# Kernel optimization log

Measured on AMD Instinct MI355X. Metric: run time of the kernel, lower is better.

Reference implementation:

```python
import jax, jax.numpy as jnp
import numpy as np
import math

NUM_SYN = 1000
NUM_MEM = 100
TAU_MIN, TAU_MAX = 10.0, 1000.0
TAU_S = 5.0
DELTA_T = 1.0
LAMBDA = 3.0

def _kappas():
    kappa_s = np.float32(np.exp(-DELTA_T / TAU_S))  # scalar (tau_s uniform)
    tau_m = np.logspace(math.log10(TAU_MIN + 1e-06), math.log10(TAU_MAX - 1e-06), NUM_MEM)
    kappa_m = np.exp(-DELTA_T / np.clip(tau_m, 1e-06, None)).astype(np.float32)
    return kappa_s, jnp.asarray(kappa_m)

def custom_tanh(x):
    return jnp.tanh(x * (2.0 / 3.0)) * 1.7159

def setup_inputs() -> dict:
    key = jax.random.key(0)
    ks = jax.random.split(key, 5)
    B, T = 128, 1024
    H = 2 * NUM_MEM  # 200
    X = jax.random.normal(ks[0], (B, T, NUM_SYN), dtype=jnp.float32)
    w_s = jnp.full((NUM_SYN,), 0.5, dtype=jnp.float32)
    W1 = jax.random.normal(ks[1], (NUM_SYN + NUM_MEM, H), dtype=jnp.float32) * 0.03
    b1 = jnp.zeros((H,), dtype=jnp.float32)
    W2 = jax.random.normal(ks[2], (H, NUM_MEM), dtype=jnp.float32) * 0.07
    b2 = jnp.zeros((NUM_MEM,), dtype=jnp.float32)
    Wy = jax.random.normal(ks[3], (NUM_MEM, 10), dtype=jnp.float32) * 0.1
    by = jnp.zeros((10,), dtype=jnp.float32)
    return {"X": X, "w_s": w_s, "W1": W1, "b1": b1, "W2": W2, "b2": b2, "Wy": Wy, "by": by}

def reference(X, w_s, W1, b1, W2, b2, Wy, by):
    kappa_s, kappa_m = _kappas()
    B = X.shape[0]
    w_s_pos = jax.nn.relu(w_s)

    def step(carry, x_t):
        s, m = carry  # s: [B, S], m: [B, M]
        s = kappa_s * s + w_s_pos * x_t
        km = kappa_m * m
        inp = jnp.concatenate([s, km], axis=-1)  # [B, S+M]
        h = jax.nn.relu(inp @ W1 + b1)
        dm = custom_tanh(h @ W2 + b2)
        m = km + LAMBDA * (1.0 - kappa_m) * dm
        y = m @ Wy + by
        return (s, m), y

    s0 = jnp.zeros((B, NUM_SYN), dtype=X.dtype)
    m0 = jnp.zeros((B, NUM_MEM), dtype=X.dtype)
    Xt = jnp.swapaxes(X, 0, 1)  # [T, B, S]
    _, ys = jax.lax.scan(step, (s0, m0), Xt)
    return jnp.swapaxes(ys, 0, 1)  # [B, T, num_output]
```

## Files before the change

### kernel.cpp

```cpp
#include <hip/hip_runtime.h>
#include <math.h>

#define SDIM 1000
#define KPAD 1024
#define HDIM 200
#define MDIM 100
#define NPAD 208
#define TSTEPS 1024
#define BATCH 128
#define MT (BATCH*TSTEPS)
#define TOTX ((size_t)MT*(size_t)SDIM)

#define Z_OFF 458752

typedef _Float16 half2_t __attribute__((ext_vector_type(2)));
typedef __attribute__((ext_vector_type(8))) short short8;
typedef __attribute__((ext_vector_type(4))) float f32x4;

static __device__ __forceinline__ unsigned short f2bf(float f) {
    unsigned u = __float_as_uint(f);
    unsigned r = 0x7fffu + ((u >> 16) & 1u);
    return (unsigned short)((u + r) >> 16);
}
static __device__ __forceinline__ float bf2f(unsigned short h) {
    return __uint_as_float((unsigned)h << 16);
}
static __device__ __forceinline__ half2_t as_h2(unsigned v) {
    union { unsigned u; half2_t h; } c; c.u = v; return c.h;
}
static __device__ __forceinline__ unsigned as_u32(half2_t h) {
    union { half2_t h; unsigned u; } c; c.h = h; return c.u;
}
static __device__ __forceinline__ half2_t pk2(float a, float b) {
    half2_t r; r[0] = (_Float16)a; r[1] = (_Float16)b; return r;
}

static __device__ __forceinline__ void wg_barrier() {
    asm volatile("s_waitcnt lgkmcnt(0)" ::: "memory");
    __builtin_amdgcn_s_barrier();
    asm volatile("" ::: "memory");
}

__global__ __launch_bounds__(256) void prep_wpt(const float* __restrict__ w_s,
                                                const float* __restrict__ W1,
                                                unsigned short* __restrict__ wpt) {
    int idx = blockIdx.x * 256 + threadIdx.x;
    int n = idx >> 10, k = idx & (KPAD - 1);
    float v = 0.f;
    if (n < HDIM && k < SDIM) {
        float ws = fmaxf(w_s[k], 0.f);
        v = ws * W1[k * HDIM + n];
    }
    wpt[idx] = f2bf(v);
}

__global__ __launch_bounds__(256) void gemm_z(const float* __restrict__ X,
                                              const unsigned short* __restrict__ wpt,
                                              unsigned short* __restrict__ Z) {
    __shared__ __align__(16) unsigned short Abuf[2][128][40];
    __shared__ __align__(16) unsigned short Bbuf[2][13][16][40];
    const int t = threadIdx.x;
    const int m0 = blockIdx.x * 128;
    const int lane = t & 63, w = t >> 6;

    f32x4 acc[2][13];
#pragma unroll
    for (int mt = 0; mt < 2; ++mt)
#pragma unroll
        for (int i = 0; i < 13; ++i) acc[mt][i] = (f32x4){0.f, 0.f, 0.f, 0.f};

    auto stageA = [&](int bsel, int k0) {
        const int row = t >> 1, half = t & 1;
        size_t g = (size_t)(m0 + row) * SDIM + (size_t)(k0 + half * 16);
        float4 f0{}, f1{}, f2{}, f3{};
        if (g + 15 < TOTX) {
            f0 = *(const float4*)(X + g);      f1 = *(const float4*)(X + g + 4);
            f2 = *(const float4*)(X + g + 8);  f3 = *(const float4*)(X + g + 12);
        }
        short8 p0, p1;
        p0[0]=(short)f2bf(f0.x); p0[1]=(short)f2bf(f0.y); p0[2]=(short)f2bf(f0.z); p0[3]=(short)f2bf(f0.w);
        p0[4]=(short)f2bf(f1.x); p0[5]=(short)f2bf(f1.y); p0[6]=(short)f2bf(f1.z); p0[7]=(short)f2bf(f1.w);
        p1[0]=(short)f2bf(f2.x); p1[1]=(short)f2bf(f2.y); p1[2]=(short)f2bf(f2.z); p1[3]=(short)f2bf(f2.w);
        p1[4]=(short)f2bf(f3.x); p1[5]=(short)f2bf(f3.y); p1[6]=(short)f2bf(f3.z); p1[7]=(short)f2bf(f3.w);
        *(short8*)&Abuf[bsel][row][half * 16]     = p0;
        *(short8*)&Abuf[bsel][row][half * 16 + 8] = p1;
    };
    auto stageB = [&](int bsel, int k0) {
#pragma unroll
        for (int j = 0; j < 4; ++j) {
            int e = t + 256 * j;
            if (e < 832) {
                int n = e >> 2, q = e & 3;
                short8 v = *(const short8*)(wpt + (size_t)n * KPAD + k0 + q * 8);
                *(short8*)&Bbuf[bsel][n >> 4][n & 15][q * 8] = v;
            }
        }
    };

    stageA(0, 0);
    stageB(0, 0);
#pragma unroll 1
    for (int it = 0; it < 32; ++it) {
        __syncthreads();
        if (it + 1 < 32) { stageA((it + 1) & 1, (it + 1) * 32); stageB((it + 1) & 1, (it + 1) * 32); }
        const int bsel = it & 1;
        const short8 av0 = *(const short8*)&Abuf[bsel][w * 32 + (lane & 15)][(lane >> 4) * 8];
        const short8 av1 = *(const short8*)&Abuf[bsel][w * 32 + 16 + (lane & 15)][(lane >> 4) * 8];
#pragma unroll
        for (int nt = 0; nt < 13; ++nt) {
            const short8 bv = *(const short8*)&Bbuf[bsel][nt][lane & 15][(lane >> 4) * 8];
            acc[0][nt] = __builtin_amdgcn_mfma_f32_16x16x32_bf16(av0, bv, acc[0][nt], 0, 0, 0);
            acc[1][nt] = __builtin_amdgcn_mfma_f32_16x16x32_bf16(av1, bv, acc[1][nt], 0, 0, 0);
        }
    }

    const int colb = lane & 15;
#pragma unroll
    for (int mt = 0; mt < 2; ++mt) {
        const int rowb = m0 + w * 32 + mt * 16 + (lane >> 4) * 4;
#pragma unroll
        for (int nt = 0; nt < 13; ++nt) {
            int col = nt * 16 + colb;
            if (col < HDIM) {
#pragma unroll
                for (int r = 0; r < 4; ++r)
                    Z[(size_t)(rowb + r) * HDIM + col] = f2bf(acc[mt][nt][r]);
            }
        }
    }
}

#define KEXP 1.9235933878519513f

__global__ __launch_bounds__(256, 1) void scan_seq(const unsigned short* __restrict__ Z,
        const float* __restrict__ W1, const float* __restrict__ b1,
        const float* __restrict__ W2, const float* __restrict__ b2,
        const float* __restrict__ Wy, const float* __restrict__ by,
        float* __restrict__ out) {
    __shared__ __align__(16) float part[2][4][104];
    __shared__ float kap_s[104], cm_s[104];

    const int t = threadIdx.x;
    const int b = blockIdx.x;
    const int w = t >> 6, lane = t & 63;
    const int n = 50 * w + lane;
    const bool hAct = lane < 50;
    const bool yAct = (w == 0) && (lane >= 50 && lane < 60);
    const int o = lane - 50;

    if (t < 104) {
        float kv = 0.f, cv = 0.f;
        if (t < MDIM) {
            double lg = 1.0000000434294482
                      + (double)t * ((2.9999999995657055 - 1.0000000434294482) / 99.0);
            double tau = exp(lg * 2.302585092994046);
            kv = (float)exp(-1.0 / tau);
            cv = 3.0f * (1.0f - kv);
        }
        kap_s[t] = kv; cm_s[t] = cv;
    }
    __syncthreads();

    half2_t w1r[50];
#pragma unroll
    for (int c = 0; c < 50; ++c) {
        float a0 = 0.f, a1 = 0.f;
        if (hAct) {
            a0 = kap_s[2 * c]     * W1[(SDIM + 2 * c)     * HDIM + n];
            a1 = kap_s[2 * c + 1] * W1[(SDIM + 2 * c + 1) * HDIM + n];
        } else if (yAct) {
            a0 = Wy[(2 * c) * 10 + o];
            a1 = Wy[(2 * c + 1) * 10 + o];
        }
        w1r[c] = pk2(a0, a1);
    }
    float base_b = hAct ? b1[n] : (yAct ? by[o] : 0.f);

    const int j0 = 2 * lane, j1 = 2 * lane + 1;
    half2_t w2r[50];
#pragma unroll
    for (int c = 0; c < 25; ++c) {
        float a00 = 0.f, a10 = 0.f, a01 = 0.f, a11 = 0.f;
        if (hAct) {
            int k0 = 50 * w + 2 * c, k1 = k0 + 1;
            a00 = W2[k0 * MDIM + j0]; a10 = W2[k1 * MDIM + j0];
            a01 = W2[k0 * MDIM + j1]; a11 = W2[k1 * MDIM + j1];
        }
        w2r[2 * c]     = pk2(a00, a10);
        w2r[2 * c + 1] = pk2(a01, a11);
    }

    float kap0 = 0.f, kap1 = 0.f, cm0 = 0.f, cm1 = 0.f, b2k0 = 0.f, b2k1 = 0.f;
    if (hAct) {
        kap0 = kap_s[j0]; kap1 = kap_s[j1];
        cm0 = cm_s[j0];   cm1 = cm_s[j1];
        b2k0 = b2[j0] * KEXP;  b2k1 = b2[j1] * KEXP;
    }

    const unsigned short* Zb = Z + (size_t)b * TSTEPS * HDIM;
    float* outb = out + (size_t)b * TSTEPS * 10;

    float u = 0.f, m0 = 0.f, m1 = 0.f;
    unsigned short zA = 0, zB = 0;
    if (hAct) { zA = Zb[n]; zB = Zb[HDIM + n]; }

    int sm[50];
#pragma unroll
    for (int c = 0; c < 50; ++c) sm[c] = 0;

    __syncthreads();

    auto stepf = [&](const int P, unsigned short& zreg, const int st) {
        u = 0.81873075307798182f * u + bf2f(zreg);
        if (hAct) {
            int stn = st + 2; stn = (stn < TSTEPS) ? stn : TSTEPS - 1;
            zreg = Zb[(size_t)stn * HDIM + n];
        }
        float d0 = base_b + u, d1 = 0.f, d2 = 0.f, d3 = 0.f;
#pragma unroll
        for (int c = 0; c < 48; c += 4) {
            d0 = __builtin_amdgcn_fdot2(w1r[c+0], as_h2((unsigned)sm[c+0]), d0, false);
            d1 = __builtin_amdgcn_fdot2(w1r[c+1], as_h2((unsigned)sm[c+1]), d1, false);
            d2 = __builtin_amdgcn_fdot2(w1r[c+2], as_h2((unsigned)sm[c+2]), d2, false);
            d3 = __builtin_amdgcn_fdot2(w1r[c+3], as_h2((unsigned)sm[c+3]), d3, false);
        }
        d0 = __builtin_amdgcn_fdot2(w1r[48], as_h2((unsigned)sm[48]), d0, false);
        d1 = __builtin_amdgcn_fdot2(w1r[49], as_h2((unsigned)sm[49]), d1, false);
        float r = (d0 + d1) + (d2 + d3);
        if (yAct && st > 0) outb[(size_t)(st - 1) * 10 + o] = r;
        float h = fmaxf(r, 0.f);

        float ho = __shfl_xor(h, 1);
        unsigned hpk = as_u32(pk2(h, ho));
        int sh[25];
#pragma unroll
        for (int c = 0; c < 25; ++c) sh[c] = __builtin_amdgcn_readlane((int)hpk, 2 * c);

        if (hAct) {
            float a00 = 0.f, a01 = 0.f, a10 = 0.f, a11 = 0.f;
#pragma unroll
            for (int c = 0; c < 24; c += 2) {
                a00 = __builtin_amdgcn_fdot2(w2r[2*c],   as_h2((unsigned)sh[c]),   a00, false);
                a10 = __builtin_amdgcn_fdot2(w2r[2*c+1], as_h2((unsigned)sh[c]),   a10, false);
                a01 = __builtin_amdgcn_fdot2(w2r[2*c+2], as_h2((unsigned)sh[c+1]), a01, false);
                a11 = __builtin_amdgcn_fdot2(w2r[2*c+3], as_h2((unsigned)sh[c+1]), a11, false);
            }
            a00 = __builtin_amdgcn_fdot2(w2r[48], as_h2((unsigned)sh[24]), a00, false);
            a10 = __builtin_amdgcn_fdot2(w2r[49], as_h2((unsigned)sh[24]), a10, false);
            *(float2*)&part[P][w][j0] = make_float2(a00 + a01, a10 + a11);
        }
        wg_barrier();

        if (hAct) {
            float2 q0 = *(const float2*)&part[P][0][j0];
            float2 q1 = *(const float2*)&part[P][1][j0];
            float2 q2 = *(const float2*)&part[P][2][j0];
            float2 q3 = *(const float2*)&part[P][3][j0];
            float s0 = (q0.x + q1.x) + (q2.x + q3.x);
            float s1 = (q0.y + q1.y) + (q2.y + q3.y);
            float e0 = __builtin_amdgcn_exp2f(fmaf(s0, KEXP, b2k0));
            float e1 = __builtin_amdgcn_exp2f(fmaf(s1, KEXP, b2k1));
            float dm0 = 1.7159f * (1.f - 2.f * __builtin_amdgcn_rcpf(e0 + 1.f));
            float dm1 = 1.7159f * (1.f - 2.f * __builtin_amdgcn_rcpf(e1 + 1.f));
            m0 = fmaf(kap0, m0, cm0 * dm0);
            m1 = fmaf(kap1, m1, cm1 * dm1);
        }
        unsigned mpk = as_u32(pk2(m0, m1));
#pragma unroll
        for (int c = 0; c < 50; ++c) sm[c] = __builtin_amdgcn_readlane((int)mpk, c);
    };

#pragma unroll 1
    for (int st = 0; st < TSTEPS; st += 2) {
        stepf(0, zA, st);
        stepf(1, zB, st + 1);
    }

    if (yAct) {
        float d0 = base_b, d1 = 0.f, d2 = 0.f, d3 = 0.f;
#pragma unroll
        for (int c = 0; c < 48; c += 4) {
            d0 = __builtin_amdgcn_fdot2(w1r[c+0], as_h2((unsigned)sm[c+0]), d0, false);
            d1 = __builtin_amdgcn_fdot2(w1r[c+1], as_h2((unsigned)sm[c+1]), d1, false);
            d2 = __builtin_amdgcn_fdot2(w1r[c+2], as_h2((unsigned)sm[c+2]), d2, false);
            d3 = __builtin_amdgcn_fdot2(w1r[c+3], as_h2((unsigned)sm[c+3]), d3, false);
        }
        d0 = __builtin_amdgcn_fdot2(w1r[48], as_h2((unsigned)sm[48]), d0, false);
        d1 = __builtin_amdgcn_fdot2(w1r[49], as_h2((unsigned)sm[49]), d1, false);
        outb[(size_t)(TSTEPS - 1) * 10 + o] = (d0 + d1) + (d2 + d3);
    }
}

extern "C" void kernel_launch(void* const* d_in, const int* in_sizes, int n_in,
                              void* d_out, int out_size, void* d_ws, size_t ws_size,
                              hipStream_t stream) {
    const float* X  = (const float*)d_in[0];
    const float* ws = (const float*)d_in[1];
    const float* W1 = (const float*)d_in[2];
    const float* b1 = (const float*)d_in[3];
    const float* W2 = (const float*)d_in[4];
    const float* b2 = (const float*)d_in[5];
    const float* Wy = (const float*)d_in[6];
    const float* by = (const float*)d_in[7];
    float* out = (float*)d_out;

    unsigned short* wpt = (unsigned short*)d_ws;
    unsigned short* Z   = (unsigned short*)((char*)d_ws + Z_OFF);

    hipLaunchKernelGGL(prep_wpt, dim3((NPAD * KPAD) / 256), dim3(256), 0, stream, ws, W1, wpt);
    hipLaunchKernelGGL(gemm_z, dim3(MT / 128), dim3(256), 0, stream, X, wpt, Z);
    hipLaunchKernelGGL(scan_seq, dim3(BATCH), dim3(256), 0, stream,
                       Z, W1, b1, W2, b2, Wy, by, out);
}
```

Measured before the change: 976.9 us.

## Halve scan workgroup to two waves, each lane computing two hidden units

The sequential scan kernel now runs with 128 threads (2 waves) instead of 256, so each lane owns two hidden units and holds twice as many packed W1/W2 weights in registers. The cross-wave partial-sum reduction drops from four to two entries, and the Z prefetch is widened to 32-bit pairs with a four-step lookahead. The intent is to make the per-step barrier and LDS reduction cheaper. In exchange, each lane does twice the dot-product work per step and register pressure rises, which lengthens the serial critical path.

```diff
diff --git a/kernel.cpp b/kernel.cpp
--- a/kernel.cpp
+++ b/kernel.cpp
@@ -131,163 +131,175 @@
 }
 
 #define KEXP 1.9235933878519513f
-
-__global__ __launch_bounds__(256, 1) void scan_seq(const unsigned short* __restrict__ Z,
+#define KS   0.81873075307798182f
+
+__global__ __launch_bounds__(128, 1) void scan_seq(const unsigned short* __restrict__ Z,
         const float* __restrict__ W1, const float* __restrict__ b1,
         const float* __restrict__ W2, const float* __restrict__ b2,
         const float* __restrict__ Wy, const float* __restrict__ by,
         float* __restrict__ out) {
-    __shared__ __align__(16) float part[2][4][104];
-    __shared__ float kap_s[104], cm_s[104];
+    __shared__ __align__(16) float part[2][2][104];
+    __shared__ float kap_s[104];
 
     const int t = threadIdx.x;
     const int b = blockIdx.x;
     const int w = t >> 6, lane = t & 63;
-    const int n = 50 * w + lane;
     const bool hAct = lane < 50;
-    const bool yAct = (w == 0) && (lane >= 50 && lane < 60);
+    const bool yAct = (w == 1) && (lane >= 50 && lane < 60);
     const int o = lane - 50;
+    const int n0 = 100 * w + 2 * lane, n1 = n0 + 1;
+    const int j0 = 2 * lane, j1 = j0 + 1;
 
     if (t < 104) {
-        float kv = 0.f, cv = 0.f;
+        float kv = 0.f;
         if (t < MDIM) {
             double lg = 1.0000000434294482
                       + (double)t * ((2.9999999995657055 - 1.0000000434294482) / 99.0);
             double tau = exp(lg * 2.302585092994046);
             kv = (float)exp(-1.0 / tau);
-            cv = 3.0f * (1.0f - kv);
-        }
-        kap_s[t] = kv; cm_s[t] = cv;
+        }
+        kap_s[t] = kv;
     }
     __syncthreads();
 
-    half2_t w1r[50];
+    half2_t w1A[50], w1B[50], w2A[50], w2B[50];
 #pragma unroll
     for (int c = 0; c < 50; ++c) {
-        float a0 = 0.f, a1 = 0.f;
+        float a0 = 0.f, a1 = 0.f, b0 = 0.f, b1v = 0.f;
+        float p0 = 0.f, p1 = 0.f, q0 = 0.f, q1 = 0.f;
         if (hAct) {
-            a0 = kap_s[2 * c]     * W1[(SDIM + 2 * c)     * HDIM + n];
-            a1 = kap_s[2 * c + 1] * W1[(SDIM + 2 * c + 1) * HDIM + n];
+            a0 = kap_s[2*c]   * W1[(SDIM + 2*c)     * HDIM + n0];
+            a1 = kap_s[2*c+1] * W1[(SDIM + 2*c + 1) * HDIM + n0];
+            b0 = kap_s[2*c]   * W1[(SDIM + 2*c)     * HDIM + n1];
+            b1v= kap_s[2*c+1] * W1[(SDIM + 2*c + 1) * HDIM + n1];
+            int k0 = 100 * w + 2 * c, k1 = k0 + 1;
+            p0 = W2[k0 * MDIM + j0]; p1 = W2[k1 * MDIM + j0];
+            q0 = W2[k0 * MDIM + j1]; q1 = W2[k1 * MDIM + j1];
         } else if (yAct) {
-            a0 = Wy[(2 * c) * 10 + o];
-            a1 = Wy[(2 * c + 1) * 10 + o];
-        }
-        w1r[c] = pk2(a0, a1);
-    }
-    float base_b = hAct ? b1[n] : (yAct ? by[o] : 0.f);
-
-    const int j0 = 2 * lane, j1 = 2 * lane + 1;
-    half2_t w2r[50];
-#pragma unroll
-    for (int c = 0; c < 25; ++c) {
-        float a00 = 0.f, a10 = 0.f, a01 = 0.f, a11 = 0.f;
-        if (hAct) {
-            int k0 = 50 * w + 2 * c, k1 = k0 + 1;
-            a00 = W2[k0 * MDIM + j0]; a10 = W2[k1 * MDIM + j0];
-            a01 = W2[k0 * MDIM + j1]; a11 = W2[k1 * MDIM + j1];
-        }
-        w2r[2 * c]     = pk2(a00, a10);
-        w2r[2 * c + 1] = pk2(a01, a11);
-    }
+            a0 = Wy[(2*c) * 10 + o];
+            a1 = Wy[(2*c + 1) * 10 + o];
+        }
+        w1A[c] = pk2(a0, a1);
+        w1B[c] = pk2(b0, b1v);
+        w2A[c] = pk2(p0, p1);
+        w2B[c] = pk2(q0, q1);
+    }
+    float bA = hAct ? b1[n0] : (yAct ? by[o] : 0.f);
+    float bB = hAct ? b1[n1] : 0.f;
 
     float kap0 = 0.f, kap1 = 0.f, cm0 = 0.f, cm1 = 0.f, b2k0 = 0.f, b2k1 = 0.f;
     if (hAct) {
         kap0 = kap_s[j0]; kap1 = kap_s[j1];
-        cm0 = cm_s[j0];   cm1 = cm_s[j1];
-        b2k0 = b2[j0] * KEXP;  b2k1 = b2[j1] * KEXP;
+        cm0 = 3.f * (1.f - kap0); cm1 = 3.f * (1.f - kap1);
+        b2k0 = b2[j0] * KEXP; b2k1 = b2[j1] * KEXP;
     }
 
     const unsigned short* Zb = Z + (size_t)b * TSTEPS * HDIM;
     float* outb = out + (size_t)b * TSTEPS * 10;
 
-    float u = 0.f, m0 = 0.f, m1 = 0.f;
-    unsigned short zA = 0, zB = 0;
-    if (hAct) { zA = Zb[n]; zB = Zb[HDIM + n]; }
-
-    int sm[50];
-#pragma unroll
-    for (int c = 0; c < 50; ++c) sm[c] = 0;
-
+    float uA = 0.f, uB = 0.f, m0 = 0.f, m1 = 0.f;
+    unsigned mpk = 0;
+    unsigned zr0 = 0, zr1 = 0, zr2 = 0, zr3 = 0;
+    if (hAct) {
+        zr0 = *(const unsigned*)(Zb + (size_t)0 * HDIM + n0);
+        zr1 = *(const unsigned*)(Zb + (size_t)1 * HDIM + n0);
+        zr2 = *(const unsigned*)(Zb + (size_t)2 * HDIM + n0);
+        zr3 = *(const unsigned*)(Zb + (size_t)3 * HDIM + n0);
+    }
     __syncthreads();
 
-    auto stepf = [&](const int P, unsigned short& zreg, const int st) {
-        u = 0.81873075307798182f * u + bf2f(zreg);
+    auto stepf = [&](const int P, unsigned& zreg, const int st) {
+        float zA = __uint_as_float(zreg << 16);
+        float zB = __uint_as_float(zreg & 0xffff0000u);
+        uA = KS * uA + zA;
+        uB = KS * uB + zB;
         if (hAct) {
-            int stn = st + 2; stn = (stn < TSTEPS) ? stn : TSTEPS - 1;
-            zreg = Zb[(size_t)stn * HDIM + n];
-        }
-        float d0 = base_b + u, d1 = 0.f, d2 = 0.f, d3 = 0.f;
+            int stn = st + 4; stn = (stn < TSTEPS) ? stn : TSTEPS - 1;
+            zreg = *(const unsigned*)(Zb + (size_t)stn * HDIM + n0);
+        }
+
+        int sm_[50];
+#pragma unroll
+        for (int c = 0; c < 50; ++c) sm_[c] = __builtin_amdgcn_readlane((int)mpk, c);
+
+        float a0 = bA + uA, a1 = 0.f, a2 = 0.f, a3 = 0.f;
+        float c0 = bB + uB, c1 = 0.f, c2 = 0.f, c3 = 0.f;
 #pragma unroll
         for (int c = 0; c < 48; c += 4) {
-            d0 = __builtin_amdgcn_fdot2(w1r[c+0], as_h2((unsigned)sm[c+0]), d0, false);
-            d1 = __builtin_amdgcn_fdot2(w1r[c+1], as_h2((unsigned)sm[c+1]), d1, false);
-            d2 = __builtin_amdgcn_fdot2(w1r[c+2], as_h2((unsigned)sm[c+2]), d2, false);
-            d3 = __builtin_amdgcn_fdot2(w1r[c+3], as_h2((unsigned)sm[c+3]), d3, false);
-        }
-        d0 = __builtin_amdgcn_fdot2(w1r[48], as_h2((unsigned)sm[48]), d0, false);
-        d1 = __builtin_amdgcn_fdot2(w1r[49], as_h2((unsigned)sm[49]), d1, false);
-        float r = (d0 + d1) + (d2 + d3);
-        if (yAct && st > 0) outb[(size_t)(st - 1) * 10 + o] = r;
-        float h = fmaxf(r, 0.f);
-
-        float ho = __shfl_xor(h, 1);
-        unsigned hpk = as_u32(pk2(h, ho));
-        int sh[25];
-#pragma unroll
-        for (int c = 0; c < 25; ++c) sh[c] = __builtin_amdgcn_readlane((int)hpk, 2 * c);
+            a0 = __builtin_amdgcn_fdot2(w1A[c+0], as_h2((unsigned)sm_[c+0]), a0, false);
+            c0 = __builtin_amdgcn_fdot2(w1B[c+0], as_h2((unsigned)sm_[c+0]), c0, false);
+            a1 = __builtin_amdgcn_fdot2(w1A[c+1], as_h2((unsigned)sm_[c+1]), a1, false);
+            c1 = __builtin_amdgcn_fdot2(w1B[c+1], as_h2((unsigned)sm_[c+1]), c1, false);
+            a2 = __builtin_amdgcn_fdot2(w1A[c+2], as_h2((unsigned)sm_[c+2]), a2, false);
+            c2 = __builtin_amdgcn_fdot2(w1B[c+2], as_h2((unsigned)sm_[c+2]), c2, false);
+            a3 = __builtin_amdgcn_fdot2(w1A[c+3], as_h2((unsigned)sm_[c+3]), a3, false);
+            c3 = __builtin_amdgcn_fdot2(w1B[c+3], as_h2((unsigned)sm_[c+3]), c3, false);
+        }
+        a0 = __builtin_amdgcn_fdot2(w1A[48], as_h2((unsigned)sm_[48]), a0, false);
+        c0 = __builtin_amdgcn_fdot2(w1B[48], as_h2((unsigned)sm_[48]), c0, false);
+        a1 = __builtin_amdgcn_fdot2(w1A[49], as_h2((unsigned)sm_[49]), a1, false);
+        c1 = __builtin_amdgcn_fdot2(w1B[49], as_h2((unsigned)sm_[49]), c1, false);
+        float rA = (a0 + a1) + (a2 + a3);
+        float rB = (c0 + c1) + (c2 + c3);
+        if (yAct && st > 0) outb[(size_t)(st - 1) * 10 + o] = rA;
+
+        unsigned hpk = as_u32(pk2(fmaxf(rA, 0.f), fmaxf(rB, 0.f)));
+        int sh_[50];
+#pragma unroll
+        for (int c = 0; c < 50; ++c) sh_[c] = __builtin_amdgcn_readlane((int)hpk, c);
+
+        float e00 = 0.f, e01 = 0.f, e10 = 0.f, e11 = 0.f;
+#pragma unroll
+        for (int c = 0; c < 50; c += 2) {
+            e00 = __builtin_amdgcn_fdot2(w2A[c],   as_h2((unsigned)sh_[c]),   e00, false);
+            e10 = __builtin_amdgcn_fdot2(w2B[c],   as_h2((unsigned)sh_[c]),   e10, false);
+            e01 = __builtin_amdgcn_fdot2(w2A[c+1], as_h2((unsigned)sh_[c+1]), e01, false);
+            e11 = __builtin_amdgcn_fdot2(w2B[c+1], as_h2((unsigned)sh_[c+1]), e11, false);
+        }
+        if (hAct)
+            *(float2*)&part[P][w][j0] = make_float2(e00 + e01, e10 + e11);
+        wg_barrier();
 
         if (hAct) {
-            float a00 = 0.f, a01 = 0.f, a10 = 0.f, a11 = 0.f;
-#pragma unroll
-            for (int c = 0; c < 24; c += 2) {
-                a00 = __builtin_amdgcn_fdot2(w2r[2*c],   as_h2((unsigned)sh[c]),   a00, false);
-                a10 = __builtin_amdgcn_fdot2(w2r[2*c+1], as_h2((unsigned)sh[c]),   a10, false);
-                a01 = __builtin_amdgcn_fdot2(w2r[2*c+2], as_h2((unsigned)sh[c+1]), a01, false);
-                a11 = __builtin_amdgcn_fdot2(w2r[2*c+3], as_h2((unsigned)sh[c+1]), a11, false);
-            }
-            a00 = __builtin_amdgcn_fdot2(w2r[48], as_h2((unsigned)sh[24]), a00, false);
-            a10 = __builtin_amdgcn_fdot2(w2r[49], as_h2((unsigned)sh[24]), a10, false);
-            *(float2*)&part[P][w][j0] = make_float2(a00 + a01, a10 + a11);
-        }
-        wg_barrier();
-
-        if (hAct) {
-            float2 q0 = *(const float2*)&part[P][0][j0];
-            float2 q1 = *(const float2*)&part[P][1][j0];
-            float2 q2 = *(const float2*)&part[P][2][j0];
-            float2 q3 = *(const float2*)&part[P][3][j0];
-            float s0 = (q0.x + q1.x) + (q2.x + q3.x);
-            float s1 = (q0.y + q1.y) + (q2.y + q3.y);
-            float e0 = __builtin_amdgcn_exp2f(fmaf(s0, KEXP, b2k0));
-            float e1 = __builtin_amdgcn_exp2f(fmaf(s1, KEXP, b2k1));
-            float dm0 = 1.7159f * (1.f - 2.f * __builtin_amdgcn_rcpf(e0 + 1.f));
-            float dm1 = 1.7159f * (1.f - 2.f * __builtin_amdgcn_rcpf(e1 + 1.f));
+            float2 p0 = *(const float2*)&part[P][0][j0];
+            float2 p1 = *(const float2*)&part[P][1][j0];
+            float s0 = p0.x + p1.x;
+            float s1 = p0.y + p1.y;
+            float E0 = __builtin_amdgcn_exp2f(fmaf(s0, KEXP, b2k0));
+            float E1 = __builtin_amdgcn_exp2f(fmaf(s1, KEXP, b2k1));
+            float dm0 = 1.7159f - 3.4318f * __builtin_amdgcn_rcpf(E0 + 1.f);
+            float dm1 = 1.7159f - 3.4318f * __builtin_amdgcn_rcpf(E1 + 1.f);
             m0 = fmaf(kap0, m0, cm0 * dm0);
             m1 = fmaf(kap1, m1, cm1 * dm1);
         }
-        unsigned mpk = as_u32(pk2(m0, m1));
-#pragma unroll
-        for (int c = 0; c < 50; ++c) sm[c] = __builtin_amdgcn_readlane((int)mpk, c);
+        mpk = as_u32(pk2(m0, m1));
     };
 
 #pragma unroll 1
-    for (int st = 0; st < TSTEPS; st += 2) {
-        stepf(0, zA, st);
-        stepf(1, zB, st + 1);
-    }
-
-    if (yAct) {
-        float d0 = base_b, d1 = 0.f, d2 = 0.f, d3 = 0.f;
-#pragma unroll
-        for (int c = 0; c < 48; c += 4) {
-            d0 = __builtin_amdgcn_fdot2(w1r[c+0], as_h2((unsigned)sm[c+0]), d0, false);
-            d1 = __builtin_amdgcn_fdot2(w1r[c+1], as_h2((unsigned)sm[c+1]), d1, false);
-            d2 = __builtin_amdgcn_fdot2(w1r[c+2], as_h2((unsigned)sm[c+2]), d2, false);
-            d3 = __builtin_amdgcn_fdot2(w1r[c+3], as_h2((unsigned)sm[c+3]), d3, false);
-        }
-        d0 = __builtin_amdgcn_fdot2(w1r[48], as_h2((unsigned)sm[48]), d0, false);
-        d1 = __builtin_amdgcn_fdot2(w1r[49], as_h2((unsigned)sm[49]), d1, false);
-        outb[(size_t)(TSTEPS - 1) * 10 + o] = (d0 + d1) + (d2 + d3);
+    for (int st = 0; st < TSTEPS; st += 4) {
+        stepf(0, zr0, st);
+        stepf(1, zr1, st + 1);
+        stepf(0, zr2, st + 2);
+        stepf(1, zr3, st + 3);
+    }
+
+    {
+        int sm_[50];
+#pragma unroll
+        for (int c = 0; c < 50; ++c) sm_[c] = __builtin_amdgcn_readlane((int)mpk, c);
+        if (yAct) {
+            float d0 = bA, d1 = 0.f, d2 = 0.f, d3 = 0.f;
+#pragma unroll
+            for (int c = 0; c < 48; c += 4) {
+                d0 = __builtin_amdgcn_fdot2(w1A[c+0], as_h2((unsigned)sm_[c+0]), d0, false);
+                d1 = __builtin_amdgcn_fdot2(w1A[c+1], as_h2((unsigned)sm_[c+1]), d1, false);
+                d2 = __builtin_amdgcn_fdot2(w1A[c+2], as_h2((unsigned)sm_[c+2]), d2, false);
+                d3 = __builtin_amdgcn_fdot2(w1A[c+3], as_h2((unsigned)sm_[c+3]), d3, false);
+            }
+            d0 = __builtin_amdgcn_fdot2(w1A[48], as_h2((unsigned)sm_[48]), d0, false);
+            d1 = __builtin_amdgcn_fdot2(w1A[49], as_h2((unsigned)sm_[49]), d1, false);
+            outb[(size_t)(TSTEPS - 1) * 10 + o] = (d0 + d1) + (d2 + d3);
+        }
     }
 }
 
@@ -309,6 +321,6 @@
 
     hipLaunchKernelGGL(prep_wpt, dim3((NPAD * KPAD) / 256), dim3(256), 0, stream, ws, W1, wpt);
     hipLaunchKernelGGL(gemm_z, dim3(MT / 128), dim3(256), 0, stream, X, wpt, Z);
-    hipLaunchKernelGGL(scan_seq, dim3(BATCH), dim3(256), 0, stream,
+    hipLaunchKernelGGL(scan_seq, dim3(BATCH), dim3(128), 0, stream,
                        Z, W1, b1, W2, b2, Wy, by, out);
 }
```

Result: slower. 1.075 ms (+10.0%).
